# Kernel tuning notes

Measured on AMD Instinct MI355X. Metric: run time of the kernel, lower is better.

Reference implementation:

```python
import jax, jax.numpy as jnp
import numpy as np

HIDDEN = 256   # opt.hidden_dim
NHEADS = 8     # forced by .view(bs, nq, -1, 8)
LVLS = 4       # opt.num_feature_levels
NQ = 300       # opt.real_num_queries
BS = 2
LVL_HWS = [(128, 128), (64, 64), (32, 32), (16, 16)]  # ceil((1024/8)/2**l)
OUT = 7        # roi_align output_size
SR = 2         # fixed sampling_ratio (torchvision default -1 is adaptive/data-dependent)
_STARTS = np.cumsum([0] + [h * w for h, w in LVL_HWS]).tolist()


def setup_inputs():
    key = jax.random.key(0)
    ks = jax.random.split(key, 20)
    def rn(i, shape, s=1.0):
        return jax.random.normal(ks[i], shape, jnp.float32) * s
    total = _STARTS[-1]
    memory = rn(0, (BS, total, HIDDEN))
    tgt = rn(1, (BS, NQ, HIDDEN))
    cxcy = jax.random.uniform(ks[2], (BS, NQ, LVLS, 2), jnp.float32)
    ltrb = jax.random.uniform(ks[3], (BS, NQ, LVLS, 4), jnp.float32) * 0.2 + 0.02
    reference = jnp.concatenate([cxcy, ltrb], axis=-1)  # (bs, nq, lvls, 6)
    level_start_index = jnp.array(_STARTS[:LVLS], jnp.int32)
    C4 = HIDDEN // 4
    params = dict(
        p1_w=rn(4, (HIDDEN, C4), 0.05), p1_b=rn(5, (C4,), 0.05),
        p2_w1=rn(6, (C4 * OUT * OUT, 256), 0.02), p2_b1=rn(7, (256,), 0.02),
        p2_w2=rn(8, (256, 512), 0.02), p2_b2=rn(9, (512,), 0.02),
        p2_w3=rn(10, (512, 512), 0.02), p2_b3=rn(11, (512,), 0.02),
        p2_w4=rn(12, (512, NHEADS * 2), 0.02), p2_b4=rn(13, (NHEADS * 2,), 0.02),
        attn1_w=rn(14, (HIDDEN, HIDDEN * NHEADS), 0.02), attn1_b=rn(15, (HIDDEN * NHEADS,), 0.02),
        attn2_w=rn(16, (HIDDEN, 1), 0.05), attn2_b=rn(17, (1,), 0.05))
    return dict(tgt=tgt, memory=memory, reference=reference,
                level_start_index=level_start_index, **params)


def _roi_align(mem2d, boxes):
    """torchvision roi_align, aligned=True, output 7x7, sampling_ratio=SR.
    mem2d: (B,C,H,W); boxes: (B,nq,4) xyxy in feature coords -> (B,nq,C,7,7)."""
    B, C, H, W = mem2d.shape
    nq = boxes.shape[1]
    fl = mem2d.reshape(B, C, H * W)
    x1, y1, x2, y2 = boxes[..., 0], boxes[..., 1], boxes[..., 2], boxes[..., 3]
    sx, sy = x1 - 0.5, y1 - 0.5                      # aligned=True half-pixel offset
    bw, bh = (x2 - x1) / OUT, (y2 - y1) / OUT
    # sample positions: bin pw, subsample ix -> pw + (ix+0.5)/SR  (pw-major order)
    t = (jnp.arange(OUT, dtype=jnp.float32)[:, None]
         + (jnp.arange(SR, dtype=jnp.float32)[None, :] + 0.5) / SR).reshape(-1)  # (S,)
    S = OUT * SR
    xs = sx[..., None] + bw[..., None] * t           # (B,nq,S)
    ys = sy[..., None] + bh[..., None] * t
    yy = jnp.broadcast_to(ys[:, :, :, None], (B, nq, S, S)).reshape(B, -1)
    xx = jnp.broadcast_to(xs[:, :, None, :], (B, nq, S, S)).reshape(B, -1)
    valid = (yy >= -1.0) & (yy <= H) & (xx >= -1.0) & (xx <= W)
    yc = jnp.clip(yy, 0.0, H - 1.0)
    xc = jnp.clip(xx, 0.0, W - 1.0)
    y0 = jnp.clip(jnp.floor(yc), 0.0, H - 2.0)
    x0 = jnp.clip(jnp.floor(xc), 0.0, W - 2.0)
    ly, lx = yc - y0, xc - x0
    y0i, x0i = y0.astype(jnp.int32), x0.astype(jnp.int32)

    def g(yi, xi):
        return jnp.take_along_axis(fl, (yi * W + xi)[:, None, :], axis=2)  # (B,C,P)

    v = (((1 - ly) * (1 - lx))[:, None] * g(y0i, x0i)
         + ((1 - ly) * lx)[:, None] * g(y0i, x0i + 1)
         + (ly * (1 - lx))[:, None] * g(y0i + 1, x0i)
         + (ly * lx)[:, None] * g(y0i + 1, x0i + 1))
    v = v * valid[:, None, :].astype(v.dtype)
    v = v.reshape(B, C, nq, OUT, SR, OUT, SR).mean(axis=(4, 6))  # bin average
    return v.transpose(0, 2, 1, 3, 4)  # (B,nq,C,7,7)


def _grid_sample(feat, gx, gy):
    """F.grid_sample bilinear, padding_mode='zeros', align_corners=False.
    feat: (N,C,H,W); gx,gy: (N,P) in [-1,1] -> (N,C,P)."""
    N, C, H, W = feat.shape
    fl = feat.reshape(N, C, H * W)
    ix = ((gx + 1.0) * W - 1.0) * 0.5
    iy = ((gy + 1.0) * H - 1.0) * 0.5
    x0, y0 = jnp.floor(ix), jnp.floor(iy)
    lx, ly = ix - x0, iy - y0
    out = jnp.zeros((N, C, gx.shape[1]), feat.dtype)
    for dy, dx, w in ((0, 0, (1 - ly) * (1 - lx)), (0, 1, (1 - ly) * lx),
                      (1, 0, ly * (1 - lx)), (1, 1, ly * lx)):
        xi, yi = x0 + dx, y0 + dy
        m = (xi >= 0) & (xi < W) & (yi >= 0) & (yi < H)
        idx = (jnp.clip(yi, 0, H - 1) * W + jnp.clip(xi, 0, W - 1)).astype(jnp.int32)
        out = out + (w * m)[:, None, :] * jnp.take_along_axis(fl, idx[:, None, :], axis=2)
    return out


def _forward(tgt, memory, ref, p1_w, p1_b, p2_w1, p2_b1, p2_w2, p2_b2,
             p2_w3, p2_b3, p2_w4, p2_b4, attn1_w, attn1_b, attn2_w, attn2_b):
    B, nq = tgt.shape[0], tgt.shape[1]
    gate = jax.nn.sigmoid((tgt @ attn1_w + attn1_b).reshape(B, nq, NHEADS, HIDDEN))
    levels = []
    for lvi in range(LVLS):
        h, w = LVL_HWS[lvi]
        s = _STARTS[lvi]
        mem2d = memory[:, s:s + h * w, :].transpose(0, 2, 1).reshape(B, HIDDEN, h, w)
        r = ref[:, :, lvi]                            # (B,nq,6): cx,cy,l,t,r,b
        cx, cy = r[..., 0], r[..., 1]
        x1 = jnp.clip(cx - r[..., 2], 0.0, 1.0) * w
        y1 = jnp.clip(cy - r[..., 3], 0.0, 1.0) * h
        x2 = jnp.clip(cx + r[..., 4], 0.0, 1.0) * w
        y2 = jnp.clip(cy + r[..., 5], 0.0, 1.0) * h
        boxes = jnp.stack([x1, y1, x2, y2], axis=-1)
        roi = _roi_align(mem2d, boxes)                # (B,nq,C,7,7)
        # point1: 1x1 conv + ReLU, then point2 MLP -> per-head sample offsets
        p = jax.nn.relu(jnp.einsum('bqchw,cd->bqdhw', roi, p1_w) + p1_b[:, None, None])
        p = p.reshape(B, nq, -1)
        p = jax.nn.relu(p @ p2_w1 + p2_b1)
        p = jax.nn.relu(p @ p2_w2 + p2_b2)
        p = jax.nn.relu(p @ p2_w3 + p2_b3)
        pts = jnp.tanh(p @ p2_w4 + p2_b4).reshape(B * nq, NHEADS, 2)
        samp = _grid_sample(roi.reshape(B * nq, HIDDEN, OUT, OUT),
                            pts[..., 0], pts[..., 1])           # (B*nq,C,8)
        samp = samp.reshape(B, nq, HIDDEN, NHEADS).transpose(0, 1, 3, 2)  # (B,nq,8,C)
        levels.append(samp * gate)
    qe = jnp.stack(levels, axis=2).reshape(B, nq, LVLS * NHEADS, HIDDEN)
    wgt = jax.nn.softmax((qe @ attn2_w + attn2_b)[..., 0], axis=-1)  # (B,nq,lvls*heads)
    return (qe * wgt[..., None]).sum(axis=-2)  # (B,nq,C)


def reference(tgt, memory, reference, level_start_index, p1_w, p1_b,
              p2_w1, p2_b1, p2_w2, p2_b2, p2_w3, p2_b3, p2_w4, p2_b4,
              attn1_w, attn1_b, attn2_w, attn2_b):
    # level_start_index is consistent with the static LVL_HWS pyramid
    return _forward(tgt, memory, reference, p1_w, p1_b, p2_w1, p2_b1,
                    p2_w2, p2_b2, p2_w3, p2_b3, p2_w4, p2_b4,
                    attn1_w, attn1_b, attn2_w, attn2_b)
```

## Files before the change

### kernel.cpp

```cpp
#include <hip/hip_runtime.h>
#include <hip/hip_bf16.h>

#define NQ     300
#define NH     8
#define HID    256
#define NLVL   4
#define NCELL  49
#define TOTAL  21760

typedef unsigned short ushort_t;
typedef __attribute__((ext_vector_type(8))) short short8;
typedef __attribute__((ext_vector_type(4))) float floatx4;
typedef __attribute__((ext_vector_type(2))) float floatx2;
typedef __attribute__((ext_vector_type(4))) unsigned int uintx4;

__device__ __forceinline__ float bfbits2f(ushort_t u) {
    union { unsigned int i; float f; } x;
    x.i = ((unsigned int)u) << 16;
    return x.f;
}
__device__ __forceinline__ ushort_t f2bfbits(float v) {
    __hip_bfloat16 h = __float2bfloat16(v);
    return *(ushort_t*)&h;
}
__device__ __forceinline__ unsigned int pack2bf(float a, float b) {
    return (unsigned int)f2bfbits(a) | ((unsigned int)f2bfbits(b) << 16);
}
__device__ __forceinline__ void split_bf(float v, ushort_t& hi, ushort_t& lo) {
    __hip_bfloat16 h = __float2bfloat16(v);
    hi = *(ushort_t*)&h;
    float hv = __bfloat162float(h);
    __hip_bfloat16 l = __float2bfloat16(v - hv);
    lo = *(ushort_t*)&l;
}

__device__ __forceinline__ floatx2 pk_fma(floatx2 a, floatx2 b, floatx2 c) {
    floatx2 d;
    asm("v_pk_fma_f32 %0, %1, %2, %3" : "=v"(d) : "v"(a), "v"(b), "v"(c));
    return d;
}
__device__ __forceinline__ floatx2 unpack2(unsigned int u) {
    union { unsigned int i; float f; } lo, hi;
    lo.i = u << 16;
    hi.i = u & 0xffff0000u;
    return (floatx2){lo.f, hi.f};
}
__device__ __forceinline__ uintx4 ld_async_b128(const ushort_t* p) {
    uintx4 d;
    asm volatile("global_load_dwordx4 %0, %1, off" : "=v"(d) : "v"(p));
    return d;
}

struct Box {
    float sx, sy, bw, bh, Wf;
    int W;
    const ushort_t* memb;
};

__device__ __forceinline__ void load_box(const float* __restrict__ refr,
                                         const ushort_t* __restrict__ mem16,
                                         int r, int lvl, int ch, Box& bx) {
    const int lvl_hw[4] = {128, 64, 32, 16};
    const int lvl_s[4]  = {0, 16384, 20480, 21504};
    const int b = r / NQ;
    bx.W  = lvl_hw[lvl];
    bx.Wf = (float)bx.W;
    const float* rp = refr + ((size_t)r * NLVL + lvl) * 6;
    float cx = rp[0], cy = rp[1];
    float dl = rp[2], dt = rp[3], dr = rp[4], db = rp[5];
    float x1 = fminf(fmaxf(cx - dl, 0.f), 1.f) * bx.Wf;
    float y1 = fminf(fmaxf(cy - dt, 0.f), 1.f) * bx.Wf;
    float x2 = fminf(fmaxf(cx + dr, 0.f), 1.f) * bx.Wf;
    float y2 = fminf(fmaxf(cy + db, 0.f), 1.f) * bx.Wf;
    bx.sx = x1 - 0.5f;
    bx.sy = y1 - 0.5f;
    bx.bw = (x2 - x1) * (1.f / 7.f);
    bx.bh = (y2 - y1) * (1.f / 7.f);
    bx.memb = mem16 + ((size_t)b * TOTAL + lvl_s[lvl]) * HID + ch;
}

__device__ __forceinline__ void tsplit_body(const float* __restrict__ W,
                                            ushort_t* __restrict__ TH,
                                            ushort_t* __restrict__ TL,
                                            int K, int N, int kb, int nb,
                                            int perm, int tid, float (*sm)[65]) {
    for (int e = tid; e < 64 * 64; e += 256) {
        int kk = e >> 6, nn = e & 63;
        int kp = kb + kk;
        int ks = perm ? ((kp & 63) * 49 + (kp >> 6)) : kp;
        sm[kk][nn] = W[(size_t)ks * N + nb + nn];
    }
    __syncthreads();
    for (int e = tid; e < 64 * 64; e += 256) {
        int nn = e >> 6, kk = e & 63;
        ushort_t h, l;
        split_bf(sm[kk][nn], h, l);
        size_t o = (size_t)(nb + nn) * K + kb + kk;
        TH[o] = h; TL[o] = l;
    }
}

__global__ __launch_bounds__(256) void k_prep(
    const float* __restrict__ tgt, ushort_t* __restrict__ tgtH, ushort_t* __restrict__ tgtL,
    const float* __restrict__ a1w, ushort_t* __restrict__ a1wTH, ushort_t* __restrict__ a1wTL,
    const float* __restrict__ w1, ushort_t* __restrict__ w1TH, ushort_t* __restrict__ w1TL,
    const float* __restrict__ w2, ushort_t* __restrict__ w2TH, ushort_t* __restrict__ w2TL,
    const float* __restrict__ w3, ushort_t* __restrict__ w3TH, ushort_t* __restrict__ w3TL,
    const float* __restrict__ p1w, ushort_t* __restrict__ p1wTH, ushort_t* __restrict__ p1wTL,
    const float* __restrict__ memory, ushort_t* __restrict__ mem16) {
    __shared__ float sm[64][65];
    const int tid = threadIdx.x;
    int b = blockIdx.x;
    if (b < 600) {
        int i = b * 256 + tid;
        ushort_t h, l;
        split_bf(tgt[i], h, l);
        tgtH[i] = h; tgtL[i] = l;
    } else if (b < 728) {
        b -= 600;
        tsplit_body(a1w, a1wTH, a1wTL, 256, 2048, (b % 4) * 64, (b / 4) * 64, 0, tid, sm);
    } else if (b < 924) {
        b -= 728;
        tsplit_body(w1, w1TH, w1TL, 3136, 256, (b % 49) * 64, (b / 49) * 64, 1, tid, sm);
    } else if (b < 956) {
        b -= 924;
        tsplit_body(w2, w2TH, w2TL, 256, 512, (b % 4) * 64, (b / 4) * 64, 0, tid, sm);
    } else if (b < 1020) {
        b -= 956;
        tsplit_body(w3, w3TH, w3TL, 512, 512, (b % 8) * 64, (b / 8) * 64, 0, tid, sm);
    } else if (b < 1024) {
        b -= 1020;
        tsplit_body(p1w, p1wTH, p1wTL, 256, 64, b * 64, 0, 0, tid, sm);
    } else {
        b -= 1024;
        size_t i = (size_t)b * 256 + tid;
        float4 v = ((const float4*)memory)[i];
        ushort4 o;
        o.x = f2bfbits(v.x); o.y = f2bfbits(v.y);
        o.z = f2bfbits(v.z); o.w = f2bfbits(v.w);
        ((ushort4*)mem16)[i] = o;
    }
}

__global__ __launch_bounds__(256) void k_w1(
    const ushort_t* __restrict__ AH, const ushort_t* __restrict__ AL,
    const ushort_t* __restrict__ WH, const ushort_t* __restrict__ WL,
    float* __restrict__ Cf, int M, int N, int K, int kchunk) {
    __shared__ ushort_t As[2][64][40];
    __shared__ ushort_t Ws[2][128][40];

    const int tid = threadIdx.x;
    const int m0 = blockIdx.x * 64, n0 = blockIdx.y * 128;
    const int wv = tid >> 6, ln = tid & 63;
    const int arow_s = tid >> 2, akc = tid & 3;
    const int wrow_s = tid >> 1, wko = (tid & 1) * 16;
    const int gm = min(m0 + arow_s, M - 1);
    const int gn = n0 + wrow_s;
    const int arow = wv * 16 + (ln & 15);
    const int koff = (ln >> 4) * 8;

    const int kb = blockIdx.z * kchunk;
    const int ke = min(K, kb + kchunk);

    floatx4 acc[8];
#pragma unroll
    for (int t = 0; t < 8; ++t) acc[t] = (floatx4){0.f, 0.f, 0.f, 0.f};

    for (int k0 = kb; k0 < ke; k0 += 32) {
        *(uint4*)&As[0][arow_s][akc * 8] = *(const uint4*)(AH + (size_t)gm * K + k0 + akc * 8);
        *(uint4*)&As[1][arow_s][akc * 8] = *(const uint4*)(AL + (size_t)gm * K + k0 + akc * 8);
        *(uint4*)&Ws[0][wrow_s][wko]     = *(const uint4*)(WH + (size_t)gn * K + k0 + wko);
        *(uint4*)&Ws[0][wrow_s][wko + 8] = *(const uint4*)(WH + (size_t)gn * K + k0 + wko + 8);
        *(uint4*)&Ws[1][wrow_s][wko]     = *(const uint4*)(WL + (size_t)gn * K + k0 + wko);
        *(uint4*)&Ws[1][wrow_s][wko + 8] = *(const uint4*)(WL + (size_t)gn * K + k0 + wko + 8);
        __syncthreads();

        short8 aH = *(short8*)&As[0][arow][koff];
        short8 aL = *(short8*)&As[1][arow][koff];
#pragma unroll
        for (int t = 0; t < 8; ++t) {
            short8 wH = *(short8*)&Ws[0][t * 16 + (ln & 15)][koff];
            short8 wL = *(short8*)&Ws[1][t * 16 + (ln & 15)][koff];
            acc[t] = __builtin_amdgcn_mfma_f32_16x16x32_bf16(aH, wH, acc[t], 0, 0, 0);
            acc[t] = __builtin_amdgcn_mfma_f32_16x16x32_bf16(aH, wL, acc[t], 0, 0, 0);
            acc[t] = __builtin_amdgcn_mfma_f32_16x16x32_bf16(aL, wH, acc[t], 0, 0, 0);
        }
        __syncthreads();
    }

    float* Cpart = Cf + (size_t)blockIdx.z * M * N;
#pragma unroll
    for (int t = 0; t < 8; ++t) {
        const int n = n0 + t * 16 + (ln & 15);
#pragma unroll
        for (int reg = 0; reg < 4; ++reg) {
            const int m = m0 + wv * 16 + (ln >> 4) * 4 + reg;
            if (m < M) Cpart[(size_t)m * N + n] = acc[t][reg];
        }
    }
}

template <int EPI, int AX, int KK, int NT>
__global__ __launch_bounds__(256) void k_wres(
    const ushort_t* __restrict__ AH, const ushort_t* __restrict__ AL,
    const ushort_t* __restrict__ WH, const ushort_t* __restrict__ WL,
    const float* __restrict__ bias, float* __restrict__ Cf,
    ushort_t* __restrict__ CH, ushort_t* __restrict__ CL,
    int M, int N, int nbm) {
    constexpr int KC = KK / 8;
    __shared__ ushort_t Wls[2 * NT * KK];

    const int tid = threadIdx.x;
    const int m0 = (blockIdx.x % nbm) * 128;
    const int n0 = (blockIdx.x / nbm) * NT;

    {
        const uint4* sH = (const uint4*)(WH + (size_t)n0 * KK);
        const uint4* sL = (const uint4*)(WL + (size_t)n0 * KK);
        uint4* d = (uint4*)Wls;
        for (int i = tid; i < NT * KC; i += 256) {
            const int nn = i / KC, kk = i % KC;
            const int sw = nn * KC + (kk ^ (nn & 7));
            d[sw] = sH[i];
            d[NT * KC + sw] = sL[i];
        }
    }
    __syncthreads();

    const int wv = tid >> 6, ln = tid & 63;
    const int koff = (ln >> 4) * 8, nidx = ln & 15;
    const size_t a0 = (size_t)min(m0 + wv * 16 + (ln & 15), M - 1) * KK;
    const size_t a1 = (size_t)min(m0 + 64 + wv * 16 + (ln & 15), M - 1) * KK;

    floatx4 acc[2][NT / 16];
#pragma unroll
    for (int s = 0; s < 2; ++s)
#pragma unroll
        for (int t = 0; t < NT / 16; ++t) acc[s][t] = (floatx4){0.f, 0.f, 0.f, 0.f};

    for (int k0 = 0; k0 < KK; k0 += 32) {
        short8 a0H = *(const short8*)(AH + a0 + k0 + koff);
        short8 a1H = *(const short8*)(AH + a1 + k0 + koff);
        short8 a0L = a0H, a1L = a1H;
        if constexpr (!AX) {
            a0L = *(const short8*)(AL + a0 + k0 + koff);
            a1L = *(const short8*)(AL + a1 + k0 + koff);
        }
        const int kc = (k0 + koff) >> 3;
#pragma unroll
        for (int t = 0; t < NT / 16; ++t) {
            const int wrow = t * 16 + nidx;
            const int swr = wrow * KC + (kc ^ (wrow & 7));
            short8 wHf = *(const short8*)((const uint4*)Wls + swr);
            short8 wLf = *(const short8*)((const uint4*)Wls + NT * KC + swr);
            acc[0][t] = __builtin_amdgcn_mfma_f32_16x16x32_bf16(a0H, wHf, acc[0][t], 0, 0, 0);
            acc[0][t] = __builtin_amdgcn_mfma_f32_16x16x32_bf16(a0H, wLf, acc[0][t], 0, 0, 0);
            if constexpr (!AX)
                acc[0][t] = __builtin_amdgcn_mfma_f32_16x16x32_bf16(a0L, wHf, acc[0][t], 0, 0, 0);
            acc[1][t] = __builtin_amdgcn_mfma_f32_16x16x32_bf16(a1H, wHf, acc[1][t], 0, 0, 0);
            acc[1][t] = __builtin_amdgcn_mfma_f32_16x16x32_bf16(a1H, wLf, acc[1][t], 0, 0, 0);
            if constexpr (!AX)
                acc[1][t] = __builtin_amdgcn_mfma_f32_16x16x32_bf16(a1L, wHf, acc[1][t], 0, 0, 0);
        }
    }

#pragma unroll
    for (int s = 0; s < 2; ++s)
#pragma unroll
        for (int t = 0; t < NT / 16; ++t) {
            const int n = n0 + t * 16 + nidx;
            const float bv = bias[n];
#pragma unroll
            for (int reg = 0; reg < 4; ++reg) {
                const int m = m0 + s * 64 + wv * 16 + (ln >> 4) * 4 + reg;
                if (m < M) {
                    float v = acc[s][t][reg] + bv;
                    if constexpr (EPI == 0) {
                        v = fmaxf(v, 0.f);
                        ushort_t h, l;
                        split_bf(v, h, l);
                        CH[(size_t)m * N + n] = h;
                        CL[(size_t)m * N + n] = l;
                    } else if constexpr (EPI == 1) {
                        Cf[(size_t)m * N + n] = fmaxf(v, 0.f);
                    } else {
                        Cf[(size_t)m * N + n] = 1.f / (1.f + expf(-v));
                    }
                }
            }
        }
}

__global__ __launch_bounds__(256) void k_h1red(
    const float* __restrict__ h1p, const float* __restrict__ b1,
    ushort_t* __restrict__ h1H, ushort_t* __restrict__ h1L) {
    const int idx = blockIdx.x * 256 + threadIdx.x;
    const int n = (idx * 4) & 255;
    float4 s = ((const float4*)h1p)[idx];
#pragma unroll
    for (int z = 1; z < 7; ++z) {
        float4 t = ((const float4*)(h1p + (size_t)z * 2400 * 256))[idx];
        s.x += t.x; s.y += t.y; s.z += t.z; s.w += t.w;
    }
    float4 bv = *(const float4*)(b1 + n);
    s.x = fmaxf(s.x + bv.x, 0.f);
    s.y = fmaxf(s.y + bv.y, 0.f);
    s.z = fmaxf(s.z + bv.z, 0.f);
    s.w = fmaxf(s.w + bv.w, 0.f);
    ushort4 H, L;
    split_bf(s.x, H.x, L.x);
    split_bf(s.y, H.y, L.y);
    split_bf(s.z, H.z, L.z);
    split_bf(s.w, H.w, L.w);
    ((ushort4*)h1H)[idx] = H;
    ((ushort4*)h1L)[idx] = L;
}

__global__ __launch_bounds__(256) void k_pts(
    const float* __restrict__ h3, const float* __restrict__ w4,
    const float* __restrict__ b4, float* __restrict__ pts) {
    __shared__ float w4s[512 * 16];
    const int tid = threadIdx.x;
    for (int i = tid; i < 512 * 16 / 4; i += 256)
        ((float4*)w4s)[i] = ((const float4*)w4)[i];
    __syncthreads();

    const int row = blockIdx.x * 4 + (tid >> 6);
    const int col = (tid >> 2) & 15;
    const int ks  = tid & 3;
    const float* hrow = h3 + (size_t)row * 512 + ks * 128;
    float part = 0.f;
    for (int k = 0; k < 128; ++k)
        part += hrow[k] * w4s[(ks * 128 + k) * 16 + col];
    part += __shfl_down(part, 2);
    part += __shfl_down(part, 1);
    if (ks == 0) pts[row * 16 + col] = tanhf(part + b4[col]);
}

__global__ __launch_bounds__(256) void k_roi(
    const ushort_t* __restrict__ mem16, const float* __restrict__ refr,
    ushort_t* __restrict__ roi) {
    const int tid  = threadIdx.x;
    const int wave = tid >> 6, lane = tid & 63;
    const int half = lane >> 5;
    const int chv  = (lane & 31) * 8;
    const int bid  = blockIdx.x;

    int lvl, r, klo, khi;
    if (bid < 1200) {
        lvl = 0; r = bid >> 1;
        klo = (bid & 1) ? 13 : 0; khi = (bid & 1) ? 25 : 13;
    } else if (bid < 2400) {
        const int t = bid - 1200;
        lvl = 1; r = t >> 1;
        klo = (t & 1) ? 13 : 0; khi = (t & 1) ? 25 : 13;
    } else if (bid < 3000) {
        lvl = 2; r = bid - 2400; klo = 0; khi = 25;
    } else {
        lvl = 3; r = bid - 3000; klo = 0; khi = 25;
    }
    const int i2 = r * 4 + lvl;

    Box bx;
    load_box(refr, mem16, r, lvl, chv, bx);
    const int rowstride = bx.W * HID;

    ushort_t* rbase = roi + (size_t)i2 * NCELL * HID + chv;

    for (int k = klo + wave; k < khi; k += 4) {
        const int cell = 2 * k + half;
        const int c = (cell < NCELL) ? cell : (NCELL - 1);
        const int ph = c / 7, pw = c % 7;

        uintx4 ld[16];
        float  w[16];
#pragma unroll
        for (int sub = 0; sub < 4; ++sub) {
            const float tys = (float)ph + ((sub >> 1) + 0.5f) * 0.5f;
            const float txs = (float)pw + ((sub & 1) + 0.5f) * 0.5f;
            const float yy = bx.sy + bx.bh * tys;
            const float xx = bx.sx + bx.bw * txs;
            const float vm = (yy >= -1.f && yy <= bx.Wf && xx <= bx.Wf && xx >= -1.f)
                             ? 0.25f : 0.f;
            const float yc  = fminf(fmaxf(yy, 0.f), bx.Wf - 1.f);
            const float xc  = fminf(fmaxf(xx, 0.f), bx.Wf - 1.f);
            const float y0f = fminf(floorf(yc), bx.Wf - 2.f);
            const float x0f = fminf(floorf(xc), bx.Wf - 2.f);
            const float ly = yc - y0f, lx = xc - x0f;
            const int   y0 = (int)y0f, x0 = (int)x0f;
            const ushort_t* p00 = bx.memb + (y0 * bx.W + x0) * HID;
            ld[sub * 4 + 0] = ld_async_b128(p00);
            ld[sub * 4 + 1] = ld_async_b128(p00 + HID);
            ld[sub * 4 + 2] = ld_async_b128(p00 + rowstride);
            ld[sub * 4 + 3] = ld_async_b128(p00 + rowstride + HID);
            const float omy = 1.f - ly, omx = 1.f - lx;
            w[sub * 4 + 0] = vm * omy * omx;
            w[sub * 4 + 1] = vm * omy * lx;
            w[sub * 4 + 2] = vm * ly  * omx;
            w[sub * 4 + 3] = vm * ly  * lx;
        }

        asm volatile("s_waitcnt vmcnt(0)" ::: "memory");
        __builtin_amdgcn_sched_barrier(0);

        floatx2 a01 = (floatx2){0.f, 0.f}, a23 = (floatx2){0.f, 0.f};
        floatx2 a45 = (floatx2){0.f, 0.f}, a67 = (floatx2){0.f, 0.f};
#pragma unroll
        for (int t = 0; t < 16; ++t) {
            const floatx2 wv2 = (floatx2){w[t], w[t]};
            a01 = pk_fma(unpack2(ld[t][0]), wv2, a01);
            a23 = pk_fma(unpack2(ld[t][1]), wv2, a23);
            a45 = pk_fma(unpack2(ld[t][2]), wv2, a45);
            a67 = pk_fma(unpack2(ld[t][3]), wv2, a67);
        }

        if (cell < NCELL) {
            uint4 o;
            o.x = pack2bf(a01.x, a01.y);
            o.y = pack2bf(a23.x, a23.y);
            o.z = pack2bf(a45.x, a45.y);
            o.w = pack2bf(a67.x, a67.y);
            *(uint4*)&rbase[c * HID] = o;
        }
    }
}

__global__ __launch_bounds__(256) void k_fuse(
    const ushort_t* __restrict__ roi, const float* __restrict__ pts,
    const float* __restrict__ gate, const float* __restrict__ w,
    const float* __restrict__ bias, float* __restrict__ out) {
    __shared__ float sm_qe[32 * HID];
    __shared__ float sm_hd[32][4];
    __shared__ float sm_l[32];
    __shared__ float sm_e[32];

    const int tid = threadIdx.x;
    const int r = blockIdx.x;

    if (tid < 32) {
        int lvl = tid >> 3, h = tid & 7;
        float gx = pts[((size_t)r * 4 + lvl) * 16 + h * 2];
        float gy = pts[((size_t)r * 4 + lvl) * 16 + h * 2 + 1];
        float ix = ((gx + 1.f) * 7.f - 1.f) * 0.5f;
        float iy = ((gy + 1.f) * 7.f - 1.f) * 0.5f;
        float x0f = floorf(ix), y0f = floorf(iy);
        sm_hd[tid][0] = x0f;
        sm_hd[tid][1] = y0f;
        sm_hd[tid][2] = ix - x0f;
        sm_hd[tid][3] = iy - y0f;
    }
    __syncthreads();

    {
        const int wid = tid >> 6;
        const int cq  = (tid & 63) * 4;
#pragma unroll
        for (int jj = 0; jj < 8; ++jj) {
            const int j = wid * 8 + jj;
            const int lvl = j >> 3, h = j & 7;
            const ushort_t* rbase = roi + ((size_t)r * 4 + lvl) * NCELL * HID + cq;
            const float x0f = sm_hd[j][0], y0f = sm_hd[j][1];
            const float lx = sm_hd[j][2], ly = sm_hd[j][3];
            const int x0 = (int)x0f, y0 = (int)y0f;
            float a0 = 0.f, a1 = 0.f, a2 = 0.f, a3 = 0.f;
#pragma unroll
            for (int dy = 0; dy < 2; ++dy) {
                const int yi = y0 + dy;
                if (yi < 0 || yi >= 7) continue;
                const float wy = dy ? ly : 1.f - ly;
#pragma unroll
                for (int dx = 0; dx < 2; ++dx) {
                    const int xi = x0 + dx;
                    if (xi < 0 || xi >= 7) continue;
                    const float wt = wy * (dx ? lx : 1.f - lx);
                    const ushort4 u = *(const ushort4*)&rbase[(yi * 7 + xi) * HID];
                    a0 += wt * bfbits2f(u.x);
                    a1 += wt * bfbits2f(u.y);
                    a2 += wt * bfbits2f(u.z);
                    a3 += wt * bfbits2f(u.w);
                }
            }
            const float4 g4 = *(const float4*)&gate[(size_t)r * 2048 + h * HID + cq];
            float4 qv;
            qv.x = a0 * g4.x; qv.y = a1 * g4.y;
            qv.z = a2 * g4.z; qv.w = a3 * g4.w;
            *(float4*)&sm_qe[j * HID + cq] = qv;
        }
    }
    __syncthreads();

    {
        const int jg = tid >> 5, lane32 = tid & 31;
#pragma unroll
        for (int p = 0; p < 4; ++p) {
            const int j = p * 8 + jg;
            float part = 0.f;
#pragma unroll
            for (int i = 0; i < 8; ++i)
                part += sm_qe[j * HID + lane32 + 32 * i] * w[lane32 + 32 * i];
            part += __shfl_down(part, 16, 32);
            part += __shfl_down(part, 8, 32);
            part += __shfl_down(part, 4, 32);
            part += __shfl_down(part, 2, 32);
            part += __shfl_down(part, 1, 32);
            if (lane32 == 0) sm_l[j] = part + bias[0];
        }
    }
    __syncthreads();
    if (tid < 32) {
        float m = -1e30f;
        for (int i = 0; i < 32; ++i) m = fmaxf(m, sm_l[i]);
        sm_e[tid] = expf(sm_l[tid] - m);
    }
    __syncthreads();
    float denom = 0.f;
    for (int i = 0; i < 32; ++i) denom += sm_e[i];
    float inv = 1.f / denom;
    float acc = 0.f;
    for (int jj = 0; jj < 32; ++jj) acc += sm_qe[jj * HID + tid] * sm_e[jj];
    out[(size_t)r * HID + tid] = acc * inv;
}

extern "C" void kernel_launch(void* const* d_in, const int* in_sizes, int n_in,
                              void* d_out, int out_size, void* d_ws, size_t ws_size,
                              hipStream_t stream) {
    const float* tgt    = (const float*)d_in[0];
    const float* memory = (const float*)d_in[1];
    const float* refr   = (const float*)d_in[2];
    const float* p1w = (const float*)d_in[4];
    const float* p1b = (const float*)d_in[5];
    const float* w1  = (const float*)d_in[6];
    const float* b1  = (const float*)d_in[7];
    const float* w2  = (const float*)d_in[8];
    const float* b2  = (const float*)d_in[9];
    const float* w3  = (const float*)d_in[10];
    const float* b3  = (const float*)d_in[11];
    const float* w4  = (const float*)d_in[12];
    const float* b4  = (const float*)d_in[13];
    const float* a1w = (const float*)d_in[14];
    const float* a1b = (const float*)d_in[15];
    const float* a2w = (const float*)d_in[16];
    const float* a2b = (const float*)d_in[17];
    float* out = (float*)d_out;

    size_t off = 0;
    auto alloc = [&](size_t bytes) {
        void* p = (char*)d_ws + off;
        off += (bytes + 255) & ~(size_t)255;
        return p;
    };
    float*    gate  = (float*)alloc((size_t)600 * 2048 * 4);
    ushort_t* mem16 = (ushort_t*)alloc((size_t)2 * TOTAL * HID * 2);
    ushort_t* roi   = (ushort_t*)alloc((size_t)2400 * NCELL * HID * 2);
    ushort_t* pHb   = (ushort_t*)alloc((size_t)2400 * 3136 * 2);
    ushort_t* pLb   = (ushort_t*)alloc((size_t)2400 * 3136 * 2);
    float*    h1p   = (float*)alloc((size_t)7 * 2400 * 256 * 4);
    ushort_t* h1H   = (ushort_t*)alloc((size_t)2400 * 256 * 2);
    ushort_t* h1L   = (ushort_t*)alloc((size_t)2400 * 256 * 2);
    ushort_t* h2H   = (ushort_t*)alloc((size_t)2400 * 512 * 2);
    ushort_t* h2L   = (ushort_t*)alloc((size_t)2400 * 512 * 2);
    float*    h3    = (float*)alloc((size_t)2400 * 512 * 4);
    float*    pts   = (float*)alloc((size_t)2400 * 16 * 4);
    ushort_t* tgtH  = (ushort_t*)alloc((size_t)600 * 256 * 2);
    ushort_t* tgtL  = (ushort_t*)alloc((size_t)600 * 256 * 2);
    ushort_t* a1wTH = (ushort_t*)alloc((size_t)2048 * 256 * 2);
    ushort_t* a1wTL = (ushort_t*)alloc((size_t)2048 * 256 * 2);
    ushort_t* w1TH  = (ushort_t*)alloc((size_t)256 * 3136 * 2);
    ushort_t* w1TL  = (ushort_t*)alloc((size_t)256 * 3136 * 2);
    ushort_t* w2TH  = (ushort_t*)alloc((size_t)512 * 256 * 2);
    ushort_t* w2TL  = (ushort_t*)alloc((size_t)512 * 256 * 2);
    ushort_t* w3TH  = (ushort_t*)alloc((size_t)512 * 512 * 2);
    ushort_t* w3TL  = (ushort_t*)alloc((size_t)512 * 512 * 2);
    ushort_t* p1wTH = (ushort_t*)alloc((size_t)64 * 256 * 2);
    ushort_t* p1wTL = (ushort_t*)alloc((size_t)64 * 256 * 2);

    hipLaunchKernelGGL(k_prep, dim3(11904), dim3(256), 0, stream,
                       tgt, tgtH, tgtL, a1w, a1wTH, a1wTL,
                       w1, w1TH, w1TL, w2, w2TH, w2TL, w3, w3TH, w3TL,
                       p1w, p1wTH, p1wTL, memory, mem16);

    hipLaunchKernelGGL((k_wres<2, 0, 256, 64>), dim3(5 * 32), dim3(256), 0, stream,
                       tgtH, tgtL, a1wTH, a1wTL, a1b, gate, (ushort_t*)0, (ushort_t*)0,
                       600, 2048, 5);
    hipLaunchKernelGGL(k_roi, dim3(3600), dim3(256), 0, stream, mem16, refr, roi);
    hipLaunchKernelGGL((k_wres<0, 1, 256, 64>), dim3(919), dim3(256), 0, stream,
                       roi, (ushort_t*)0, p1wTH, p1wTL, p1b, (float*)0, pHb, pLb,
                       2400 * NCELL, 64, 919);
    hipLaunchKernelGGL(k_w1, dim3(38, 2, 7), dim3(256), 0, stream,
                       pHb, pLb, w1TH, w1TL, h1p, 2400, 256, 3136, 448);
    hipLaunchKernelGGL(k_h1red, dim3(600), dim3(256), 0, stream, h1p, b1, h1H, h1L);
    hipLaunchKernelGGL((k_wres<0, 0, 256, 64>), dim3(19 * 8), dim3(256), 0, stream,
                       h1H, h1L, w2TH, w2TL, b2, (float*)0, h2H, h2L, 2400, 512, 19);
    hipLaunchKernelGGL((k_wres<1, 0, 512, 32>), dim3(19 * 16), dim3(256), 0, stream,
                       h2H, h2L, w3TH, w3TL, b3, h3, (ushort_t*)0, (ushort_t*)0,
                       2400, 512, 19);
    hipLaunchKernelGGL(k_pts, dim3(600), dim3(256), 0, stream, h3, w4, b4, pts);
    hipLaunchKernelGGL(k_fuse, dim3(600), dim3(256), 0, stream,
                       roi, pts, gate, a2w, a2b, out);
}
```

Baseline: 318.2 us.

## Fuse ROI-align sampling with the p1 projection GEMM in one kernel

Merges the ROI-align kernel and the following p1 linear layer (with ReLU and hi/lo bf16 split) into a single kernel. Each block computes one box-level's 49x256 ROI tile, stages it in swizzled shared memory, and then runs MFMA against the p1 weights. This removes a kernel launch and the global reread of the ROI tensor by the separate GEMM. In exchange it drops the finer split of large-level boxes across two blocks, so there are fewer blocks and some load imbalance, and it uses extra shared memory per block. The A operand only uses the high bf16 part of the ROI values.

Measured after the change: 373.6 us. +17.4%, slower.

```diff
diff --git a/kernel.cpp b/kernel.cpp
--- a/kernel.cpp
+++ b/kernel.cpp
@@ -337,29 +337,21 @@
     if (ks == 0) pts[row * 16 + col] = tanhf(part + b4[col]);
 }
 
-__global__ __launch_bounds__(256) void k_roi(
+__global__ __launch_bounds__(256) void k_roip1(
     const ushort_t* __restrict__ mem16, const float* __restrict__ refr,
-    ushort_t* __restrict__ roi) {
+    ushort_t* __restrict__ roi,
+    const ushort_t* __restrict__ WH, const ushort_t* __restrict__ WL,
+    const float* __restrict__ bias,
+    ushort_t* __restrict__ CH, ushort_t* __restrict__ CL) {
+    __shared__ uint4 As4[64 * 32];
+
     const int tid  = threadIdx.x;
     const int wave = tid >> 6, lane = tid & 63;
     const int half = lane >> 5;
     const int chv  = (lane & 31) * 8;
-    const int bid  = blockIdx.x;
-
-    int lvl, r, klo, khi;
-    if (bid < 1200) {
-        lvl = 0; r = bid >> 1;
-        klo = (bid & 1) ? 13 : 0; khi = (bid & 1) ? 25 : 13;
-    } else if (bid < 2400) {
-        const int t = bid - 1200;
-        lvl = 1; r = t >> 1;
-        klo = (t & 1) ? 13 : 0; khi = (t & 1) ? 25 : 13;
-    } else if (bid < 3000) {
-        lvl = 2; r = bid - 2400; klo = 0; khi = 25;
-    } else {
-        lvl = 3; r = bid - 3000; klo = 0; khi = 25;
-    }
-    const int i2 = r * 4 + lvl;
+    const int lvl  = blockIdx.x & 3;
+    const int r    = blockIdx.x >> 2;
+    const int i2   = r * 4 + lvl;
 
     Box bx;
     load_box(refr, mem16, r, lvl, chv, bx);
@@ -367,7 +359,7 @@
 
     ushort_t* rbase = roi + (size_t)i2 * NCELL * HID + chv;
 
-    for (int k = klo + wave; k < khi; k += 4) {
+    for (int k = wave; k < 25; k += 4) {
         const int cell = 2 * k + half;
         const int c = (cell < NCELL) ? cell : (NCELL - 1);
         const int ph = c / 7, pw = c % 7;
@@ -421,6 +413,47 @@
             o.z = pack2bf(a45.x, a45.y);
             o.w = pack2bf(a67.x, a67.y);
             *(uint4*)&rbase[c * HID] = o;
+            As4[c * 32 + ((lane & 31) ^ (c & 7))] = o;
+        }
+    }
+    __syncthreads();
+
+    const int koff = (lane >> 4) * 8;
+    const int nidx = lane & 15;
+    const int arow = wave * 16 + nidx;
+
+    floatx4 acc[4];
+#pragma unroll
+    for (int t = 0; t < 4; ++t) acc[t] = (floatx4){0.f, 0.f, 0.f, 0.f};
+
+    for (int k0 = 0; k0 < 256; k0 += 32) {
+        const int chunk = (k0 >> 3) + (lane >> 4);
+        short8 aH = *(short8*)&As4[arow * 32 + (chunk ^ (arow & 7))];
+#pragma unroll
+        for (int t = 0; t < 4; ++t) {
+            const int wrow = t * 16 + nidx;
+            short8 wHf = *(const short8*)(WH + (size_t)wrow * 256 + k0 + koff);
+            short8 wLf = *(const short8*)(WL + (size_t)wrow * 256 + k0 + koff);
+            acc[t] = __builtin_amdgcn_mfma_f32_16x16x32_bf16(aH, wHf, acc[t], 0, 0, 0);
+            acc[t] = __builtin_amdgcn_mfma_f32_16x16x32_bf16(aH, wLf, acc[t], 0, 0, 0);
+        }
+    }
+
+#pragma unroll
+    for (int t = 0; t < 4; ++t) {
+        const int n = t * 16 + nidx;
+        const float bv = bias[n];
+#pragma unroll
+        for (int reg = 0; reg < 4; ++reg) {
+            const int mt = wave * 16 + (lane >> 4) * 4 + reg;
+            if (mt < NCELL) {
+                float v = fmaxf(acc[t][reg] + bv, 0.f);
+                ushort_t h, l;
+                split_bf(v, h, l);
+                const size_t m = (size_t)i2 * NCELL + mt;
+                CH[m * 64 + n] = h;
+                CL[m * 64 + n] = l;
+            }
         }
     }
 }
@@ -582,10 +615,8 @@
     hipLaunchKernelGGL((k_wres<2, 0, 256, 64>), dim3(5 * 32), dim3(256), 0, stream,
                        tgtH, tgtL, a1wTH, a1wTL, a1b, gate, (ushort_t*)0, (ushort_t*)0,
                        600, 2048, 5);
-    hipLaunchKernelGGL(k_roi, dim3(3600), dim3(256), 0, stream, mem16, refr, roi);
-    hipLaunchKernelGGL((k_wres<0, 1, 256, 64>), dim3(919), dim3(256), 0, stream,
-                       roi, (ushort_t*)0, p1wTH, p1wTL, p1b, (float*)0, pHb, pLb,
-                       2400 * NCELL, 64, 919);
+    hipLaunchKernelGGL(k_roip1, dim3(2400), dim3(256), 0, stream,
+                       mem16, refr, roi, p1wTH, p1wTL, p1b, pHb, pLb);
     hipLaunchKernelGGL(k_w1, dim3(38, 2, 7), dim3(256), 0, stream,
                        pHb, pLb, w1TH, w1TL, h1p, 2400, 256, 3136, 448);
     hipLaunchKernelGGL(k_h1red, dim3(600), dim3(256), 0, stream, h1p, b1, h1H, h1L);
```
